# Optimization experiments

Hardware: AMD Instinct MI355X
Metric: run time of the kernel (lower is better)

The kernel has to match this reference:

```python
import jax, jax.numpy as jnp
import numpy as np
import math

D = 1024
H = 8
HD = D // H
TEMP = math.sqrt(D)
EPS = 1e-5

def _layernorm(x, g, b):
    mu = jnp.mean(x, axis=-1, keepdims=True)
    var = jnp.var(x, axis=-1, keepdims=True)
    return (x - mu) * jax.lax.rsqrt(var + EPS) * g + b

def setup_inputs() -> dict:
    key = jax.random.key(0)
    ks = jax.random.split(key, 8)
    B, Lq, Lk = 4, 2048, 2048
    Q = jax.random.normal(ks[0], (B, Lq, D), dtype=jnp.float32)
    K = jax.random.normal(ks[1], (B, Lk, D), dtype=jnp.float32)
    V = jax.random.normal(ks[2], (B, Lk, D), dtype=jnp.float32)
    Wq = jax.random.normal(ks[3], (D, D), dtype=jnp.float32) * 0.02
    Wk = jax.random.normal(ks[4], (D, D), dtype=jnp.float32) * 0.02
    Wv = jax.random.normal(ks[5], (D, D), dtype=jnp.float32) * 0.02
    Wo = jax.random.normal(ks[6], (D, D), dtype=jnp.float32) * 0.02
    pre_g = jnp.ones((D,), jnp.float32)
    pre_b = jnp.zeros((D,), jnp.float32)
    ln_g = jnp.ones((D,), jnp.float32)
    ln_b = jnp.zeros((D,), jnp.float32)
    return {"Q": Q, "K": K, "V": V, "Wq": Wq, "Wk": Wk, "Wv": Wv, "Wo": Wo,
            "pre_g": pre_g, "pre_b": pre_b, "ln_g": ln_g, "ln_b": ln_b}

def reference(Q, K, V, Wq, Wk, Wv, Wo, pre_g, pre_b, ln_g, ln_b):
    B, Lq, _ = Q.shape
    Lk = K.shape[1]
    # pre-LN on Q and K only (V untouched, as in original)
    Qn = _layernorm(Q, pre_g, pre_b)
    Kn = _layernorm(K, pre_g, pre_b)
    q = (Qn @ Wq).reshape(B, Lq, H, HD)
    k = (Kn @ Wk).reshape(B, Lk, H, HD)
    v = (V @ Wv).reshape(B, Lk, H, HD)
    scores = jnp.einsum('bqhd,bkhd->bhqk', q, k) / TEMP
    scores = jnp.clip(scores, -10000.0, 10000.0)
    A = jax.nn.softmax(scores, axis=-1)  # dropout = identity in eval
    O = jnp.einsum('bhqk,bkhd->bqhd', A, v).reshape(B, Lq, D)
    O = _layernorm(O, ln_g, ln_b)
    O = O + jax.nn.gelu(O @ Wo, approximate=False)  # residual branch
    return O
```

## Files before the change

kernel.cpp:

```cpp
#include <hip/hip_runtime.h>
#include <math.h>

typedef unsigned short u16;
typedef __bf16 bf16x8 __attribute__((ext_vector_type(8)));
typedef float f32x4 __attribute__((ext_vector_type(4)));

union B8u { uint4 u; bf16x8 v; u16 s[8]; };

__device__ __forceinline__ u16 f2bf(float f){
  unsigned u = __float_as_uint(f);
  u += 0x7fffu + ((u >> 16) & 1u);
  return (u16)(u >> 16);
}
__device__ __forceinline__ bf16x8 ld8(const u16* p){
  B8u x; x.u = *(const uint4*)p; return x.v;
}
__device__ __forceinline__ void glds16(const u16* g, u16* l){
  __builtin_amdgcn_global_load_lds(
      (const __attribute__((address_space(1))) void*)g,
      (__attribute__((address_space(3))) void*)l, 16, 0, 0);
}

__global__ void wcast_k(const float* __restrict__ Wq, const float* __restrict__ Wk,
                        const float* __restrict__ Wv, const float* __restrict__ Wo,
                        u16* __restrict__ Tq, u16* __restrict__ Tk,
                        u16* __restrict__ Tv, u16* __restrict__ To){
  const float* W; u16* T;
  switch(blockIdx.z){
    case 0: W = Wq; T = Tq; break;
    case 1: W = Wk; T = Tk; break;
    case 2: W = Wv; T = Tv; break;
    default: W = Wo; T = To; break;
  }
  __shared__ u16 tile[32][33];
  int tx = threadIdx.x & 31, ty = threadIdx.x >> 5;
  int n0 = blockIdx.x * 32, k0 = blockIdx.y * 32;
  for(int i = ty; i < 32; i += 8)
    tile[i][tx] = f2bf(W[(size_t)(k0 + i) * 1024 + n0 + tx]);
  __syncthreads();
  for(int i = ty; i < 32; i += 8)
    T[(size_t)(n0 + i) * 1024 + k0 + tx] = tile[tx][i];
}

__device__ __forceinline__ void ln_core(const float* __restrict__ X,
                                        u16* __restrict__ Y, float* __restrict__ Yf,
                                        const float* __restrict__ g,
                                        const float* __restrict__ bb,
                                        int doLN, int row, int t, float* red){
  float4 v = ((const float4*)(X + (size_t)row * 1024))[t];
  float o0 = v.x, o1 = v.y, o2 = v.z, o3 = v.w;
  if(doLN){
    float s  = o0 + o1 + o2 + o3;
    float ss = o0*o0 + o1*o1 + o2*o2 + o3*o3;
    for(int o = 32; o > 0; o >>= 1){
      s  += __shfl_down(s,  o, 64);
      ss += __shfl_down(ss, o, 64);
    }
    if((t & 63) == 0){ red[t >> 6] = s; red[4 + (t >> 6)] = ss; }
    __syncthreads();
    s  = red[0] + red[1] + red[2] + red[3];
    ss = red[4] + red[5] + red[6] + red[7];
    float mu  = s * (1.f/1024.f);
    float var = ss * (1.f/1024.f) - mu*mu;
    float rs  = rsqrtf(var + 1e-5f);
    float4 gg = ((const float4*)g)[t];
    float4 bv = ((const float4*)bb)[t];
    o0 = (o0 - mu) * rs * gg.x + bv.x;
    o1 = (o1 - mu) * rs * gg.y + bv.y;
    o2 = (o2 - mu) * rs * gg.z + bv.z;
    o3 = (o3 - mu) * rs * gg.w + bv.w;
  }
  if(Yf){
    float4 w; w.x=o0; w.y=o1; w.z=o2; w.w=o3;
    ((float4*)(Yf + (size_t)row * 1024))[t] = w;
  }
  ushort4 u;
  u.x = f2bf(o0); u.y = f2bf(o1); u.z = f2bf(o2); u.w = f2bf(o3);
  ((ushort4*)(Y + (size_t)row * 1024))[t] = u;
}

__global__ void ln3_cast(const float* __restrict__ Q, const float* __restrict__ K,
                         const float* __restrict__ V,
                         u16* __restrict__ QN, u16* __restrict__ KN, u16* __restrict__ VB,
                         const float* __restrict__ g, const float* __restrict__ bb){
  __shared__ float red[8];
  const float* X; u16* Y; int doLN = 1;
  switch(blockIdx.y){
    case 0: X = Q; Y = QN; break;
    case 1: X = K; Y = KN; break;
    default: X = V; Y = VB; doLN = 0; break;
  }
  ln_core(X, Y, nullptr, g, bb, doLN, blockIdx.x, threadIdx.x, red);
}

__global__ void ln_post(const float* __restrict__ X, u16* __restrict__ Y,
                        float* __restrict__ Yf,
                        const float* __restrict__ g, const float* __restrict__ bb){
  __shared__ float red[8];
  ln_core(X, Y, Yf, g, bb, 1, blockIdx.x, threadIdx.x, red);
}

template<int MODE>
__device__ __forceinline__ void gemm_core(
  const u16* __restrict__ A, const u16* __restrict__ Bt,
  u16* __restrict__ Obf, float* __restrict__ Of32, const float* __restrict__ Resid,
  int m0, int n0, int ldC, float oscale, u16* as, u16* bs)
{
  const int K = 1024;
  int t = threadIdx.x;
  int wave = t >> 6, lane = t & 63, quad = lane >> 4, l16 = lane & 15;
  int wm = (wave >> 1) * 64, wn = (wave & 1) * 64;
  int srow = t >> 3;
  f32x4 acc[4][4] = {};
  for(int k0 = 0; k0 < K; k0 += 64){
    __syncthreads();
    for(int p = 0; p < 4; p++){
      int r = p*32 + srow;
      int c = (t & 7) ^ (r & 7);
      glds16(A  + (size_t)(m0 + r) * K + k0 + c*8, as + p*2048 + wave*512);
      glds16(Bt + (size_t)(n0 + r) * K + k0 + c*8, bs + p*2048 + wave*512);
    }
    __syncthreads();
    bf16x8 af[2][4], bfr[2][4];
    for(int kk = 0; kk < 2; kk++)
      for(int mt = 0; mt < 4; mt++){
        int ra = wm + mt*16 + l16;
        af[kk][mt]  = ld8(&as[ra*64 + (((kk*4 + quad) ^ (ra & 7)) * 8)]);
        int rb = wn + mt*16 + l16;
        bfr[kk][mt] = ld8(&bs[rb*64 + (((kk*4 + quad) ^ (rb & 7)) * 8)]);
      }
    for(int kk = 0; kk < 2; kk++)
      for(int mt = 0; mt < 4; mt++)
        for(int nt = 0; nt < 4; nt++)
          acc[mt][nt] = __builtin_amdgcn_mfma_f32_16x16x32_bf16(af[kk][mt], bfr[kk][nt], acc[mt][nt], 0, 0, 0);
  }
  for(int mt = 0; mt < 4; mt++)
    for(int nt = 0; nt < 4; nt++){
      int col = n0 + wn + nt*16 + l16;
      for(int r = 0; r < 4; r++){
        int row = m0 + wm + mt*16 + quad*4 + r;
        size_t idx = (size_t)row * ldC + col;
        float v = acc[mt][nt][r];
        if(MODE == 0){
          Obf[idx] = f2bf(v * oscale);
        } else {
          float ge = 0.5f * v * (1.0f + erff(v * 0.70710678118f));
          Of32[idx] = Resid[idx] + ge;
        }
      }
    }
}

__global__ __launch_bounds__(256,3) void qkv_gemm(
  const u16* __restrict__ QN, const u16* __restrict__ KN, const u16* __restrict__ VB,
  const u16* __restrict__ WTq, const u16* __restrict__ WTk, const u16* __restrict__ WTv,
  u16* __restrict__ QP, u16* __restrict__ KP, u16* __restrict__ VT, float qscale)
{
  __shared__ u16 as[128*64];
  __shared__ u16 bs[128*64];
  int bx = blockIdx.x;
  int z = bx % 3, id = bx / 3;
  if(z == 0){
    gemm_core<0>(QN, WTq, QP, nullptr, nullptr, (id >> 3)*128, (id & 7)*128, 1024, qscale, as, bs);
  } else if(z == 1){
    gemm_core<0>(KN, WTk, KP, nullptr, nullptr, (id >> 3)*128, (id & 7)*128, 1024, 1.0f, as, bs);
  } else {
    gemm_core<0>(WTv, VB, VT, nullptr, nullptr, (id & 7)*128, (id >> 3)*128, 8192, 1.0f, as, bs);
  }
}

__global__ __launch_bounds__(256,3) void out_gemm(
  const u16* __restrict__ A, const u16* __restrict__ Bt,
  float* __restrict__ Of32, const float* __restrict__ Resid)
{
  __shared__ u16 as[128*64];
  __shared__ u16 bs[128*64];
  gemm_core<1>(A, Bt, nullptr, Of32, Resid, blockIdx.x*128, blockIdx.y*128, 1024, 1.0f, as, bs);
}

__global__ __launch_bounds__(512,4) void flash_k(
  const u16* __restrict__ Qp, const u16* __restrict__ Kp, const u16* __restrict__ VT,
  float* __restrict__ Oout)
{
  __shared__ u16 ks[64*128];
  __shared__ u16 vts[128*64];
  __shared__ u16 ps[128][72];
  int t = threadIdx.x, wave = t >> 6, lane = t & 63, quad = lane >> 4, l16 = lane & 15;
  int l = blockIdx.x;
  int xcd = l & 7, i = l >> 3;
  int bh = xcd + 8 * (i & 3);
  int qt = i >> 2;
  int b = bh >> 3, h = bh & 7;
  size_t rowbase = (size_t)b * 2048;
  int colbase = h * 128;
  int wq = wave * 16;

  bf16x8 aq[4];
  {
    const u16* qrow = Qp + (rowbase + qt*128 + wq + l16) * 1024 + colbase + quad*8;
    for(int kk = 0; kk < 4; kk++) aq[kk] = ld8(qrow + kk*32);
  }

  float l_i[4] = {};
  f32x4 oacc[8] = {};

  int krow = t >> 4;
  int kchunk = lane & 15;
  int vrow = t >> 3;
  int vchunk = lane & 7;

  for(int p = 0; p < 2; p++){
    int kr = p*32 + krow;
    int ck = kchunk ^ (kr & 15);
    glds16(Kp + (rowbase + kr) * 1024 + colbase + ck*8, ks + p*4096 + wave*512);
  }
  for(int p = 0; p < 2; p++){
    int vr = p*64 + vrow;
    int cv = vchunk ^ (vr & 7);
    glds16(VT + (size_t)(colbase + vr) * 8192 + rowbase + cv*8,
           vts + p*4096 + wave*512);
  }
  __syncthreads();

  for(int kt = 0; kt < 2048; kt += 64){
    f32x4 s[4] = {};
    __builtin_amdgcn_s_setprio(1);
    for(int ct = 0; ct < 4; ct++)
      for(int kk = 0; kk < 4; kk++){
        bf16x8 bb = ld8(&ks[(ct*16 + l16)*128 + (((kk*4 + quad) ^ l16) * 8)]);
        s[ct] = __builtin_amdgcn_mfma_f32_16x16x32_bf16(aq[kk], bb, s[ct], 0, 0, 0);
      }
    __builtin_amdgcn_s_setprio(0);
    for(int ct = 0; ct < 4; ct++)
      for(int r = 0; r < 4; r++)
        s[ct][r] = __builtin_amdgcn_exp2f(s[ct][r]);
    for(int r = 0; r < 4; r++){
      l_i[r] += (s[0][r] + s[1][r]) + (s[2][r] + s[3][r]);
      for(int ct = 0; ct < 4; ct++){
        unsigned u = __float_as_uint(s[ct][r]) + 0x8000u;
        ps[wq + quad*4 + r][ct*16 + l16] = (u16)(u >> 16);
      }
    }
    __syncthreads();
    if(kt + 64 < 2048){
      for(int p = 0; p < 2; p++){
        int kr = p*32 + krow;
        int ck = kchunk ^ (kr & 15);
        glds16(Kp + (rowbase + kt + 64 + kr) * 1024 + colbase + ck*8,
               ks + p*4096 + wave*512);
      }
    }
    bf16x8 pa0 = ld8(&ps[wq + l16][quad*8]);
    bf16x8 pa1 = ld8(&ps[wq + l16][32 + quad*8]);
    __builtin_amdgcn_s_setprio(1);
    for(int dt = 0; dt < 8; dt++){
      int vrw = (dt*16 + l16)*64;
      int r7 = l16 & 7;
      bf16x8 b0 = ld8(&vts[vrw + ((quad ^ r7) * 8)]);
      oacc[dt] = __builtin_amdgcn_mfma_f32_16x16x32_bf16(pa0, b0, oacc[dt], 0, 0, 0);
      bf16x8 b1 = ld8(&vts[vrw + (((4 + quad) ^ r7) * 8)]);
      oacc[dt] = __builtin_amdgcn_mfma_f32_16x16x32_bf16(pa1, b1, oacc[dt], 0, 0, 0);
    }
    __builtin_amdgcn_s_setprio(0);
    __syncthreads();
    if(kt + 64 < 2048){
      for(int p = 0; p < 2; p++){
        int vr = p*64 + vrow;
        int cv = vchunk ^ (vr & 7);
        glds16(VT + (size_t)(colbase + vr) * 8192 + rowbase + kt + 64 + cv*8,
               vts + p*4096 + wave*512);
      }
    }
  }
  float rinv[4];
  for(int r = 0; r < 4; r++){
    float lv = l_i[r];
    for(int o = 1; o < 16; o <<= 1) lv += __shfl_xor(lv, o, 64);
    rinv[r] = 1.f / lv;
  }
  for(int dt = 0; dt < 8; dt++){
    int col = colbase + dt*16 + l16;
    for(int r = 0; r < 4; r++){
      size_t row = rowbase + qt*128 + wq + quad*4 + r;
      Oout[row * 1024 + col] = oacc[dt][r] * rinv[r];
    }
  }
}

extern "C" void kernel_launch(void* const* d_in, const int* in_sizes, int n_in,
                              void* d_out, int out_size, void* d_ws, size_t ws_size,
                              hipStream_t stream){
  (void)in_sizes; (void)n_in; (void)out_size; (void)ws_size;
  const float* Q    = (const float*)d_in[0];
  const float* K    = (const float*)d_in[1];
  const float* V    = (const float*)d_in[2];
  const float* Wq   = (const float*)d_in[3];
  const float* Wk   = (const float*)d_in[4];
  const float* Wv   = (const float*)d_in[5];
  const float* Wo   = (const float*)d_in[6];
  const float* pre_g = (const float*)d_in[7];
  const float* pre_b = (const float*)d_in[8];
  const float* ln_g  = (const float*)d_in[9];
  const float* ln_b  = (const float*)d_in[10];
  float* Out = (float*)d_out;
  char* ws = (char*)d_ws;
  const size_t MB = 1024 * 1024;
  u16* WTq = (u16*)(ws + 0*MB);
  u16* WTk = (u16*)(ws + 2*MB);
  u16* WTv = (u16*)(ws + 4*MB);
  u16* WTo = (u16*)(ws + 6*MB);
  u16* QN  = (u16*)(ws + 8*MB);
  u16* KN  = (u16*)(ws + 24*MB);
  u16* VB  = (u16*)(ws + 40*MB);
  u16* QP  = (u16*)(ws + 56*MB);
  u16* KP  = (u16*)(ws + 72*MB);
  u16* VT  = (u16*)(ws + 88*MB);
  float* OLN  = (float*)(ws + 8*MB);
  u16*   OLNb = (u16*)(ws + 40*MB);

  const float qscale = 0.03125f * 1.44269504089f;

  wcast_k<<<dim3(32,32,4), 256, 0, stream>>>(Wq,Wk,Wv,Wo, WTq,WTk,WTv,WTo);
  ln3_cast<<<dim3(8192,3), 256, 0, stream>>>(Q, K, V, QN, KN, VB, pre_g, pre_b);
  qkv_gemm<<<1536, 256, 0, stream>>>(QN, KN, VB, WTq, WTk, WTv, QP, KP, VT, qscale);
  flash_k<<<512, 512, 0, stream>>>(QP, KP, VT, Out);
  ln_post<<<8192, 256, 0, stream>>>(Out, OLNb, OLN, ln_g, ln_b);
  out_gemm<<<dim3(64,8), 256, 0, stream>>>(OLNb, WTo, Out, OLN);
}
```

Baseline: 356.6 us.

## Double-buffer K/V tiles in flash kernel and remap QKV GEMM blocks

The attention kernel now keeps two K and V tile buffers in LDS and prefetches the next tile before computing the current one, which leaves a single barrier per step. The P tile loses its padding and uses an XOR swizzle instead. QKV GEMM block indices are remapped so that each XCD handles a contiguous range of tiles, improving cache locality. The larger LDS footprint reduces how many attention blocks can reside on a CU at once.

```diff
diff --git a/kernel.cpp b/kernel.cpp
--- a/kernel.cpp
+++ b/kernel.cpp
@@ -159,7 +159,8 @@
   __shared__ u16 as[128*64];
   __shared__ u16 bs[128*64];
   int bx = blockIdx.x;
-  int z = bx % 3, id = bx / 3;
+  int w = (bx >> 3) + 192 * (bx & 7);
+  int z = w / 512, id = w - z * 512;
   if(z == 0){
     gemm_core<0>(QN, WTq, QP, nullptr, nullptr, (id >> 3)*128, (id & 7)*128, 1024, qscale, as, bs);
   } else if(z == 1){
@@ -182,9 +183,9 @@
   const u16* __restrict__ Qp, const u16* __restrict__ Kp, const u16* __restrict__ VT,
   float* __restrict__ Oout)
 {
-  __shared__ u16 ks[64*128];
-  __shared__ u16 vts[128*64];
-  __shared__ u16 ps[128][72];
+  __shared__ u16 ks[2*64*128];
+  __shared__ u16 vts[2*128*64];
+  __shared__ u16 ps[128*64];
   int t = threadIdx.x, wave = t >> 6, lane = t & 63, quad = lane >> 4, l16 = lane & 15;
   int l = blockIdx.x;
   int xcd = l & 7, i = l >> 3;
@@ -213,8 +214,6 @@
     int kr = p*32 + krow;
     int ck = kchunk ^ (kr & 15);
     glds16(Kp + (rowbase + kr) * 1024 + colbase + ck*8, ks + p*4096 + wave*512);
-  }
-  for(int p = 0; p < 2; p++){
     int vr = p*64 + vrow;
     int cv = vchunk ^ (vr & 7);
     glds16(VT + (size_t)(colbase + vr) * 8192 + rowbase + cv*8,
@@ -222,12 +221,28 @@
   }
   __syncthreads();
 
-  for(int kt = 0; kt < 2048; kt += 64){
+  auto step = [&](int CUR, int KTV) {
+    const u16* ksc = ks  + CUR*8192;
+    const u16* vtc = vts + CUR*8192;
+    if(KTV + 64 < 2048){
+      u16* ksn = ks  + (1-CUR)*8192;
+      u16* vtn = vts + (1-CUR)*8192;
+      for(int p = 0; p < 2; p++){
+        int kr = p*32 + krow;
+        int ck = kchunk ^ (kr & 15);
+        glds16(Kp + (rowbase + KTV + 64 + kr) * 1024 + colbase + ck*8,
+               ksn + p*4096 + wave*512);
+        int vr = p*64 + vrow;
+        int cv = vchunk ^ (vr & 7);
+        glds16(VT + (size_t)(colbase + vr) * 8192 + rowbase + KTV + 64 + cv*8,
+               vtn + p*4096 + wave*512);
+      }
+    }
     f32x4 s[4] = {};
     __builtin_amdgcn_s_setprio(1);
     for(int ct = 0; ct < 4; ct++)
       for(int kk = 0; kk < 4; kk++){
-        bf16x8 bb = ld8(&ks[(ct*16 + l16)*128 + (((kk*4 + quad) ^ l16) * 8)]);
+        bf16x8 bb = ld8(&ksc[(ct*16 + l16)*128 + (((kk*4 + quad) ^ l16) * 8)]);
         s[ct] = __builtin_amdgcn_mfma_f32_16x16x32_bf16(aq[kk], bb, s[ct], 0, 0, 0);
       }
     __builtin_amdgcn_s_setprio(0);
@@ -236,42 +251,33 @@
         s[ct][r] = __builtin_amdgcn_exp2f(s[ct][r]);
     for(int r = 0; r < 4; r++){
       l_i[r] += (s[0][r] + s[1][r]) + (s[2][r] + s[3][r]);
+      int prow = wq + quad*4 + r;
+      int rs = prow & 7;
       for(int ct = 0; ct < 4; ct++){
         unsigned u = __float_as_uint(s[ct][r]) + 0x8000u;
-        ps[wq + quad*4 + r][ct*16 + l16] = (u16)(u >> 16);
-      }
-    }
-    __syncthreads();
-    if(kt + 64 < 2048){
-      for(int p = 0; p < 2; p++){
-        int kr = p*32 + krow;
-        int ck = kchunk ^ (kr & 15);
-        glds16(Kp + (rowbase + kt + 64 + kr) * 1024 + colbase + ck*8,
-               ks + p*4096 + wave*512);
-      }
-    }
-    bf16x8 pa0 = ld8(&ps[wq + l16][quad*8]);
-    bf16x8 pa1 = ld8(&ps[wq + l16][32 + quad*8]);
+        ps[prow*64 + (((ct*2 + (l16 >> 3)) ^ rs) * 8) + (l16 & 7)] = (u16)(u >> 16);
+      }
+    }
+    bf16x8 pa0 = ld8(&ps[(wq + l16)*64 + ((quad ^ (l16 & 7)) * 8)]);
+    bf16x8 pa1 = ld8(&ps[(wq + l16)*64 + (((4 + quad) ^ (l16 & 7)) * 8)]);
     __builtin_amdgcn_s_setprio(1);
     for(int dt = 0; dt < 8; dt++){
       int vrw = (dt*16 + l16)*64;
       int r7 = l16 & 7;
-      bf16x8 b0 = ld8(&vts[vrw + ((quad ^ r7) * 8)]);
+      bf16x8 b0 = ld8(&vtc[vrw + ((quad ^ r7) * 8)]);
       oacc[dt] = __builtin_amdgcn_mfma_f32_16x16x32_bf16(pa0, b0, oacc[dt], 0, 0, 0);
-      bf16x8 b1 = ld8(&vts[vrw + (((4 + quad) ^ r7) * 8)]);
+      bf16x8 b1 = ld8(&vtc[vrw + (((4 + quad) ^ r7) * 8)]);
       oacc[dt] = __builtin_amdgcn_mfma_f32_16x16x32_bf16(pa1, b1, oacc[dt], 0, 0, 0);
     }
     __builtin_amdgcn_s_setprio(0);
     __syncthreads();
-    if(kt + 64 < 2048){
-      for(int p = 0; p < 2; p++){
-        int vr = p*64 + vrow;
-        int cv = vchunk ^ (vr & 7);
-        glds16(VT + (size_t)(colbase + vr) * 8192 + rowbase + kt + 64 + cv*8,
-               vts + p*4096 + wave*512);
-      }
-    }
-  }
+  };
+
+  for(int kt = 0; kt < 2048; kt += 128){
+    step(0, kt);
+    step(1, kt + 64);
+  }
+
   float rinv[4];
   for(int r = 0; r < 4; r++){
     float lv = l_i[r];
```

Result: faster. 347.4 us (-2.6%).

## Double-buffer K/V tiles and split key dimension across waves in flash kernel

Applied to the files above, without the earlier changes.

The flash attention kernel now double-buffers K and V tiles in shared memory, issuing the next tile's loads at the top of each iteration so they overlap compute and one barrier per iteration is removed. Each wave now handles 32 query rows and one half of each 64-key tile, sharing each loaded B fragment across two MFMAs, and the two key-halves are combined through LDS at the end. The P buffer gets an XOR swizzle instead of padding. The QKV GEMM block-to-work mapping is remapped so that consecutive blocks on an XCD work on the same matrix. This costs more shared memory, which may lower occupancy, and adds a final reduction pass through LDS.

```diff
diff --git a/kernel.cpp b/kernel.cpp
--- a/kernel.cpp
+++ b/kernel.cpp
@@ -11,6 +11,9 @@
   unsigned u = __float_as_uint(f);
   u += 0x7fffu + ((u >> 16) & 1u);
   return (u16)(u >> 16);
+}
+__device__ __forceinline__ u16 f2bf_fast(float f){
+  return (u16)((__float_as_uint(f) + 0x8000u) >> 16);
 }
 __device__ __forceinline__ bf16x8 ld8(const u16* p){
   B8u x; x.u = *(const uint4*)p; return x.v;
@@ -159,7 +162,8 @@
   __shared__ u16 as[128*64];
   __shared__ u16 bs[128*64];
   int bx = blockIdx.x;
-  int z = bx % 3, id = bx / 3;
+  int w = (bx >> 3) + 192 * (bx & 7);
+  int z = w / 512, id = w - z * 512;
   if(z == 0){
     gemm_core<0>(QN, WTq, QP, nullptr, nullptr, (id >> 3)*128, (id & 7)*128, 1024, qscale, as, bs);
   } else if(z == 1){
@@ -182,9 +186,10 @@
   const u16* __restrict__ Qp, const u16* __restrict__ Kp, const u16* __restrict__ VT,
   float* __restrict__ Oout)
 {
-  __shared__ u16 ks[64*128];
-  __shared__ u16 vts[128*64];
-  __shared__ u16 ps[128][72];
+  __shared__ __align__(16) u16 smem[40960];
+  u16* ks  = smem;
+  u16* vts = smem + 16384;
+  u16* ps  = smem + 32768;
   int t = threadIdx.x, wave = t >> 6, lane = t & 63, quad = lane >> 4, l16 = lane & 15;
   int l = blockIdx.x;
   int xcd = l & 7, i = l >> 3;
@@ -193,96 +198,112 @@
   int b = bh >> 3, h = bh & 7;
   size_t rowbase = (size_t)b * 2048;
   int colbase = h * 128;
-  int wq = wave * 16;
-
-  bf16x8 aq[4];
+  int wq = (wave & 3) * 32;
+  int kb = (wave >> 2) * 32;
+  int khq = (kb >> 3) + quad;
+
+  bf16x8 aq[2][4];
+  for(int m = 0; m < 2; m++){
+    const u16* qrow = Qp + (rowbase + qt*128 + wq + m*16 + l16) * 1024 + colbase + quad*8;
+    for(int kk = 0; kk < 4; kk++) aq[m][kk] = ld8(qrow + kk*32);
+  }
+
+  float l_i[2][4] = {};
+  f32x4 oacc[2][8] = {};
+
+  int krow = t >> 4;
+  int kchunk = t & 15;
+  int vrow = t >> 3;
+  int vchunk = t & 7;
+
+  const u16* kp = Kp + (rowbase + krow) * 1024 + colbase + (kchunk ^ (krow & 15)) * 8;
+  const u16* vt = VT + (size_t)(colbase + vrow) * 8192 + rowbase + (vchunk ^ (vrow & 7)) * 8;
+
   {
-    const u16* qrow = Qp + (rowbase + qt*128 + wq + l16) * 1024 + colbase + quad*8;
-    for(int kk = 0; kk < 4; kk++) aq[kk] = ld8(qrow + kk*32);
-  }
-
-  float l_i[4] = {};
-  f32x4 oacc[8] = {};
-
-  int krow = t >> 4;
-  int kchunk = lane & 15;
-  int vrow = t >> 3;
-  int vchunk = lane & 7;
-
-  for(int p = 0; p < 2; p++){
-    int kr = p*32 + krow;
-    int ck = kchunk ^ (kr & 15);
-    glds16(Kp + (rowbase + kr) * 1024 + colbase + ck*8, ks + p*4096 + wave*512);
-  }
-  for(int p = 0; p < 2; p++){
-    int vr = p*64 + vrow;
-    int cv = vchunk ^ (vr & 7);
-    glds16(VT + (size_t)(colbase + vr) * 8192 + rowbase + cv*8,
-           vts + p*4096 + wave*512);
+    u16* kd = ks + wave*512;
+    u16* vd = vts + wave*512;
+    glds16(kp, kd);          glds16(kp + 32768, kd + 4096);
+    glds16(vt, vd);          glds16(vt + 524288, vd + 4096);
+    kp += 65536; vt += 64;
   }
   __syncthreads();
 
   for(int kt = 0; kt < 2048; kt += 64){
-    f32x4 s[4] = {};
-    __builtin_amdgcn_s_setprio(1);
-    for(int ct = 0; ct < 4; ct++)
+    int buf = (kt >> 6) & 1;
+    const u16* ksc = ks + buf*8192;
+    const u16* vtc = vts + buf*8192;
+    if(kt + 64 < 2048){
+      u16* kd = ks + (buf^1)*8192 + wave*512;
+      u16* vd = vts + (buf^1)*8192 + wave*512;
+      glds16(kp, kd);          glds16(kp + 32768, kd + 4096);
+      glds16(vt, vd);          glds16(vt + 524288, vd + 4096);
+      kp += 65536; vt += 64;
+    }
+    for(int ct = 0; ct < 2; ct++){
+      f32x4 s0 = {}, s1 = {};
+      __builtin_amdgcn_s_setprio(1);
       for(int kk = 0; kk < 4; kk++){
-        bf16x8 bb = ld8(&ks[(ct*16 + l16)*128 + (((kk*4 + quad) ^ l16) * 8)]);
-        s[ct] = __builtin_amdgcn_mfma_f32_16x16x32_bf16(aq[kk], bb, s[ct], 0, 0, 0);
-      }
-    __builtin_amdgcn_s_setprio(0);
-    for(int ct = 0; ct < 4; ct++)
-      for(int r = 0; r < 4; r++)
-        s[ct][r] = __builtin_amdgcn_exp2f(s[ct][r]);
-    for(int r = 0; r < 4; r++){
-      l_i[r] += (s[0][r] + s[1][r]) + (s[2][r] + s[3][r]);
-      for(int ct = 0; ct < 4; ct++){
-        unsigned u = __float_as_uint(s[ct][r]) + 0x8000u;
-        ps[wq + quad*4 + r][ct*16 + l16] = (u16)(u >> 16);
-      }
-    }
-    __syncthreads();
-    if(kt + 64 < 2048){
-      for(int p = 0; p < 2; p++){
-        int kr = p*32 + krow;
-        int ck = kchunk ^ (kr & 15);
-        glds16(Kp + (rowbase + kt + 64 + kr) * 1024 + colbase + ck*8,
-               ks + p*4096 + wave*512);
-      }
-    }
-    bf16x8 pa0 = ld8(&ps[wq + l16][quad*8]);
-    bf16x8 pa1 = ld8(&ps[wq + l16][32 + quad*8]);
+        bf16x8 bb = ld8(&ksc[(kb + ct*16 + l16)*128 + (((kk*4 + quad) ^ l16) * 8)]);
+        s0 = __builtin_amdgcn_mfma_f32_16x16x32_bf16(aq[0][kk], bb, s0, 0, 0, 0);
+        s1 = __builtin_amdgcn_mfma_f32_16x16x32_bf16(aq[1][kk], bb, s1, 0, 0, 0);
+      }
+      __builtin_amdgcn_s_setprio(0);
+      for(int r = 0; r < 4; r++){
+        s0[r] = __builtin_amdgcn_exp2f(s0[r]);
+        s1[r] = __builtin_amdgcn_exp2f(s1[r]);
+      }
+      int ch = (kb >> 3) + ct*2 + (l16 >> 3);
+      for(int r = 0; r < 4; r++){
+        l_i[0][r] += s0[r];
+        l_i[1][r] += s1[r];
+        int pr0 = wq + quad*4 + r;
+        int pr1 = pr0 + 16;
+        int cx = (ch ^ (pr0 & 7)) * 8 + (l16 & 7);
+        ps[pr0*64 + cx] = f2bf_fast(s0[r]);
+        ps[pr1*64 + cx] = f2bf_fast(s1[r]);
+      }
+    }
+    bf16x8 pa0 = ld8(&ps[(wq + l16)*64      + ((khq ^ (l16 & 7)) * 8)]);
+    bf16x8 pa1 = ld8(&ps[(wq + 16 + l16)*64 + ((khq ^ (l16 & 7)) * 8)]);
     __builtin_amdgcn_s_setprio(1);
     for(int dt = 0; dt < 8; dt++){
-      int vrw = (dt*16 + l16)*64;
-      int r7 = l16 & 7;
-      bf16x8 b0 = ld8(&vts[vrw + ((quad ^ r7) * 8)]);
-      oacc[dt] = __builtin_amdgcn_mfma_f32_16x16x32_bf16(pa0, b0, oacc[dt], 0, 0, 0);
-      bf16x8 b1 = ld8(&vts[vrw + (((4 + quad) ^ r7) * 8)]);
-      oacc[dt] = __builtin_amdgcn_mfma_f32_16x16x32_bf16(pa1, b1, oacc[dt], 0, 0, 0);
+      bf16x8 bb = ld8(&vtc[(dt*16 + l16)*64 + ((khq ^ (l16 & 7)) * 8)]);
+      oacc[0][dt] = __builtin_amdgcn_mfma_f32_16x16x32_bf16(pa0, bb, oacc[0][dt], 0, 0, 0);
+      oacc[1][dt] = __builtin_amdgcn_mfma_f32_16x16x32_bf16(pa1, bb, oacc[1][dt], 0, 0, 0);
     }
     __builtin_amdgcn_s_setprio(0);
     __syncthreads();
-    if(kt + 64 < 2048){
-      for(int p = 0; p < 2; p++){
-        int vr = p*64 + vrow;
-        int cv = vchunk ^ (vr & 7);
-        glds16(VT + (size_t)(colbase + vr) * 8192 + rowbase + kt + 64 + cv*8,
-               vts + p*4096 + wave*512);
-      }
-    }
-  }
-  float rinv[4];
-  for(int r = 0; r < 4; r++){
-    float lv = l_i[r];
-    for(int o = 1; o < 16; o <<= 1) lv += __shfl_xor(lv, o, 64);
-    rinv[r] = 1.f / lv;
-  }
-  for(int dt = 0; dt < 8; dt++){
-    int col = colbase + dt*16 + l16;
-    for(int r = 0; r < 4; r++){
-      size_t row = rowbase + qt*128 + wq + quad*4 + r;
-      Oout[row * 1024 + col] = oacc[dt][r] * rinv[r];
+  }
+
+  float* o_lds = (float*)smem;
+  float* l_lds = (float*)(smem + 33792);
+  if(kb == 0){
+    for(int m = 0; m < 2; m++)
+      for(int r = 0; r < 4; r++){
+        int row = wq + m*16 + quad*4 + r;
+        l_lds[row*16 + l16] = l_i[m][r];
+        for(int dt = 0; dt < 8; dt++)
+          o_lds[row*132 + dt*16 + l16] = oacc[m][dt][r];
+      }
+  }
+  __syncthreads();
+  if(kb != 0){
+    for(int m = 0; m < 2; m++){
+      float rinv[4];
+      for(int r = 0; r < 4; r++){
+        int row = wq + m*16 + quad*4 + r;
+        float lv = l_i[m][r] + l_lds[row*16 + l16];
+        for(int o = 1; o < 16; o <<= 1) lv += __shfl_xor(lv, o, 64);
+        rinv[r] = 1.f / lv;
+      }
+      for(int dt = 0; dt < 8; dt++){
+        int col = colbase + dt*16 + l16;
+        for(int r = 0; r < 4; r++){
+          int row = wq + m*16 + quad*4 + r;
+          size_t grow = rowbase + qt*128 + row;
+          Oout[grow * 1024 + col] = (oacc[m][dt][r] + o_lds[row*132 + dt*16 + l16]) * rinv[r];
+        }
+      }
     }
   }
 }
```

After: 403.8 us. +13.2%, slower.
